# Optimization experiments

Hardware: AMD Instinct MI355X
Metric: run time of the kernel (lower is better)

## Reference

```python
import jax, jax.numpy as jnp
import numpy as np
from jax import lax

B, V_ECC, V_ERR, T, C = 8192, 16, 12, 25, 32
F_IN = C * T           # 800 = temporal_out * tf_num
G = 64                 # gcn_out
H2 = 256               # hidden_size * 2
EHR_DIM, EHR_OUT = 64, 64

def _lhat(V):
    # bidirectional ring graph; PyG ChebConv sym-norm with lambda_max=2.0:
    # L_hat = (2/lmax) * (I - D^-1/2 A D^-1/2) - I = -D^-1/2 A D^-1/2
    i = np.arange(V)
    src = np.concatenate([i, (i + 1) % V])
    dst = np.concatenate([(i + 1) % V, i])
    A = np.zeros((V, V), np.float32)
    A[src, dst] = 1.0
    deg = A.sum(1)
    dinv = np.where(deg > 0, deg ** -0.5, 0.0).astype(np.float32)
    return jnp.asarray(-(dinv[:, None] * A * dinv[None, :]))

LHAT_ECC = _lhat(V_ECC)
LHAT_ERR = _lhat(V_ERR)

def setup_inputs():
    key = jax.random.key(0)
    ks = jax.random.split(key, 23)
    n = lambda k, s: jax.random.normal(k, s, jnp.float32) * 0.02
    return {
        "ecc": jax.random.normal(ks[0], (B, V_ECC, T), jnp.float32),
        "err": jax.random.normal(ks[1], (B, V_ERR, T), jnp.float32),
        "ehr": jax.random.normal(ks[2], (B, EHR_DIM), jnp.float32),
        "wt_ecc": n(ks[3], (C, 1, 3)), "bt_ecc": n(ks[4], (C,)),
        "wt_err": n(ks[5], (C, 1, 3)), "bt_err": n(ks[6], (C,)),
        "W0_ecc": n(ks[7], (F_IN, G)), "W1_ecc": n(ks[8], (F_IN, G)), "b_ecc": n(ks[9], (G,)),
        "W0_err": n(ks[10], (F_IN, G)), "W1_err": n(ks[11], (F_IN, G)), "b_err": n(ks[12], (G,)),
        "Wp_ecc": n(ks[13], (V_ECC * G, H2)), "bp_ecc": n(ks[14], (H2,)),
        "Wp_err": n(ks[15], (V_ERR * G, H2)), "bp_err": n(ks[16], (H2,)),
        "Wa": n(ks[17], (H2, 1)), "ba": n(ks[18], (1,)),
        "We": n(ks[19], (EHR_DIM, EHR_OUT)), "be": n(ks[20], (EHR_OUT,)),
        "Wf2": n(ks[21], (H2 + EHR_OUT, 1)), "bf2": n(ks[22], (1,)),
    }

def _temporal(x, w, b):
    # x: [B, V, T]; Conv1d(1 -> C, k=3, padding=1) per node, then flatten (C, T)
    bb, v, t = x.shape
    y = lax.conv_general_dilated(x.reshape(bb * v, 1, t), w, (1,), "SAME",
                                 dimension_numbers=("NCH", "OIH", "NCH"))
    y = y + b[None, :, None]
    return y.reshape(bb, v, -1)        # [B, V, C*T]

def _cheb(x, lhat, w0, w1, b):
    # K=2 ChebConv: out = T0(x)@W0 + T1(x)@W1 + b, T1 = L_hat x (batched over B)
    tx1 = jnp.einsum("uv,bvd->bud", lhat, x)
    return x @ w0 + tx1 @ w1 + b

def reference(ecc, err, ehr, wt_ecc, bt_ecc, wt_err, bt_err,
              W0_ecc, W1_ecc, b_ecc, W0_err, W1_err, b_err,
              Wp_ecc, bp_ecc, Wp_err, bp_err, Wa, ba, We, be, Wf2, bf2):
    bsz = ecc.shape[0]
    ecc_f = _temporal(ecc, wt_ecc, bt_ecc)                    # [B,16,800]
    err_f = _temporal(err, wt_err, bt_err)                    # [B,12,800]
    ecc_out = _cheb(ecc_f, LHAT_ECC, W0_ecc, W1_ecc, b_ecc)   # [B,16,64]
    err_out = _cheb(err_f, LHAT_ERR, W0_err, W1_err, b_err)   # [B,12,64]
    ecc_g = ecc_out.reshape(bsz, -1) @ Wp_ecc + bp_ecc        # [B,256]
    err_g = err_out.reshape(bsz, -1) @ Wp_err + bp_err        # [B,256]
    attn = jax.nn.sigmoid(jnp.tanh(ecc_g + err_g) @ Wa + ba)  # [B,1]
    fused = attn * ecc_g + (1.0 - attn) * err_g
    ehr_p = jax.nn.relu(ehr @ We + be)                        # dropout = identity (eval)
    combined = jnp.concatenate([fused, ehr_p], axis=1)        # [B,320]
    x = jax.nn.relu(combined)
    return jax.nn.sigmoid(x @ Wf2 + bf2)                      # [B,1]
```

## Files before the change

kernel.cpp:

```cpp
#include <hip/hip_runtime.h>
#include <math.h>

#define B_TOT 8192
#define KE 400
#define KR 300
#define MEP 416
#define MRP 320

#define ROWS 16

#define SXE_LD 424
#define SXR_LD 328
#define SEH_LD 72
#define A_BYTES (ROWS * (SXE_LD + SXR_LD + SEH_LD) * 2)

#define OFF_BE 0
#define OFF_BR 4096
#define U_AET 14336
#define U_ART (U_AET + 256 * MEP)
#define U_WET (U_ART + 256 * MRP)

typedef __attribute__((ext_vector_type(8))) short short8;
typedef __attribute__((ext_vector_type(4))) float floatx4;

__device__ __forceinline__ float sigmoidf_(float x) { return 1.f / (1.f + __expf(-x)); }
__device__ __forceinline__ float tanhf_(float x) { float e = __expf(2.f * x); return (e - 1.f) / (e + 1.f); }
__device__ __forceinline__ unsigned short f2bf(float x) {
    unsigned u = __float_as_uint(x);
    u += 0x7fffu + ((u >> 16) & 1u);
    return (unsigned short)(u >> 16);
}
__device__ __forceinline__ void gload_lds16(const unsigned short* g, unsigned short* l) {
    __builtin_amdgcn_global_load_lds(
        (const __attribute__((address_space(1))) void*)g,
        (__attribute__((address_space(3))) void*)l, 16, 0, 0);
}

__global__ __launch_bounds__(256) void fold_all2(
    const float* __restrict__ wt_ecc, const float* __restrict__ bt_ecc,
    const float* __restrict__ wt_err, const float* __restrict__ bt_err,
    const float* __restrict__ W0_ecc, const float* __restrict__ W1_ecc, const float* __restrict__ b_ecc,
    const float* __restrict__ W0_err, const float* __restrict__ W1_err, const float* __restrict__ b_err,
    const float* __restrict__ Wp_ecc, const float* __restrict__ bp_ecc,
    const float* __restrict__ Wp_err, const float* __restrict__ bp_err,
    const float* __restrict__ We,
    float* __restrict__ wsf, unsigned short* __restrict__ wsu)
{
    const int blk = blockIdx.x;
    const int tid = threadIdx.x;
    const int cq = tid >> 6;
    const int g  = tid & 63;

    __shared__ float red0[4][64];
    __shared__ float red1[4][64];
    __shared__ float sw0[64];
    __shared__ float sw1[64];

    if (blk < MEP + MRP) {
        const int kb = (blk & 7) * 92 + (blk >> 3);
        const bool is_err = (kb >= MEP);
        const int k  = is_err ? kb - MEP : kb;
        const int KK = is_err ? KR : KE;
        const int MP = is_err ? MRP : MEP;
        const int nv = is_err ? 12 : 16;
        const float* wt = is_err ? wt_err : wt_ecc;
        const float* W0 = is_err ? W0_err : W0_ecc;
        const float* W1 = is_err ? W1_err : W1_ecc;
        const float* Wp = is_err ? Wp_err : Wp_ecc;
        const int ubase = is_err ? U_ART : U_AET;

        float s = 0.f;
        if (k < KK) {
            const int v = k / 25, tin = k % 25;
            const int t0 = tin > 0 ? tin - 1 : 0;
            const int t1 = tin < 24 ? tin + 1 : 24;
            float s0 = 0.f, s1 = 0.f;
            #pragma unroll
            for (int c8 = 0; c8 < 8; ++c8) {
                const int c = cq * 8 + c8;
                for (int t = t0; t <= t1; ++t) {
                    const int kk = tin - t + 1;
                    const float w = wt[c * 3 + kk];
                    const int ct = (c * 25 + t) * 64 + g;
                    s0 = fmaf(w, W0[ct], s0);
                    s1 = fmaf(w, W1[ct], s1);
                }
            }
            red0[cq][g] = s0;
            red1[cq][g] = s1;
            __syncthreads();
            if (tid < 64)
                sw0[g] = red0[0][g] + red0[1][g] + red0[2][g] + red0[3][g];
            else if (tid < 128)
                sw1[tid - 64] = red1[0][tid - 64] + red1[1][tid - 64] + red1[2][tid - 64] + red1[3][tid - 64];
            __syncthreads();

            const int vp = (v + 1) % nv;
            const int vm = (v + nv - 1) % nv;
            const int h = tid;
            #pragma unroll 4
            for (int gg = 0; gg < 64; ++gg) {
                s = fmaf(sw0[gg], Wp[(v * 64 + gg) * 256 + h], s);
                s = fmaf(-0.5f * sw1[gg], Wp[(vp * 64 + gg) * 256 + h] + Wp[(vm * 64 + gg) * 256 + h], s);
            }
        }
        wsu[ubase + (size_t)tid * MP + k] = f2bf(s);
    } else if (blk < MEP + MRP + 28) {
        const int cb = blk - (MEP + MRP);
        const bool is_err = (cb >= 16);
        const int i = is_err ? cb - 16 : cb;
        const float* bt = is_err ? bt_err : bt_ecc;
        const float* W0 = is_err ? W0_err : W0_ecc;
        const float* W1 = is_err ? W1_err : W1_ecc;
        const float* bb = is_err ? b_err : b_ecc;
        const float* Wp = is_err ? Wp_err : Wp_ecc;
        const float* bp = is_err ? bp_err : bp_ecc;

        float s = 0.f;
        #pragma unroll
        for (int c8 = 0; c8 < 8; ++c8) {
            const int c = cq * 8 + c8;
            const float btc = bt[c];
            #pragma unroll
            for (int t = 0; t < 25; ++t) {
                const int ct = (c * 25 + t) * 64 + g;
                s = fmaf(btc, W0[ct] - W1[ct], s);
            }
        }
        red0[cq][g] = s;
        __syncthreads();
        if (tid < 64)
            sw0[g] = bb[g] + red0[0][g] + red0[1][g] + red0[2][g] + red0[3][g];
        __syncthreads();

        const int h = tid;
        float p = (i == 0) ? bp[h] : 0.f;
        #pragma unroll 4
        for (int jj = 0; jj < 64; ++jj) {
            const int j = i * 64 + jj;
            p = fmaf(sw0[j & 63], Wp[(size_t)j * 256 + h], p);
        }
        wsf[(is_err ? OFF_BR : OFF_BE) + i * 256 + h] = p;
    } else {
        for (int it = 0; it < 16; ++it) {
            const int idx = it * 256 + tid;
            const int e = idx >> 6, d = idx & 63;
            wsu[U_WET + e * 64 + d] = f2bf(We[d * 64 + e]);
        }
    }
}

__global__ __launch_bounds__(256, 2) void fused_main(
    const float* __restrict__ ecc, const float* __restrict__ err, const float* __restrict__ ehr,
    const float* __restrict__ wsf, const unsigned short* __restrict__ wsu,
    const float* __restrict__ Wa, const float* __restrict__ ba,
    const float* __restrict__ be_, const float* __restrict__ Wf2, const float* __restrict__ bf2,
    float* __restrict__ out)
{
    const unsigned short* awt_e = wsu + U_AET;
    const unsigned short* awt_r = wsu + U_ART;
    const unsigned short* wet   = wsu + U_WET;
    const float* biasE = wsf + OFF_BE;
    const float* biasR = wsf + OFF_BR;

    __shared__ __align__(16) char smem[A_BYTES + 3 * 16384];
    unsigned short* sxe = (unsigned short*)smem;
    unsigned short* sxr = sxe + ROWS * SXE_LD;
    unsigned short* seh = sxr + ROWS * SXR_LD;
    unsigned short* bbuf = (unsigned short*)(smem + A_BYTES);
    float* pa_part = (float*)smem;
    float* at_arr  = pa_part + 64;
    float* po_part = at_arr + 16;

    const int tid = threadIdx.x;
    const int row0 = blockIdx.x * ROWS;
    const int wv = tid >> 6, lane = tid & 63;
    const int lm = lane & 15, lq = lane >> 4;
    const int n0 = wv * 64;

    const int srow = lane >> 2;
    const int scol = ((lane & 3) ^ ((lane >> 3) & 3)) * 8;
    const unsigned short* geb = awt_e + (size_t)(n0 + srow) * MEP + scol;
    const unsigned short* grb = awt_r + (size_t)(n0 + srow) * MRP + scol;

    {
        unsigned short* ld0 = bbuf + 0 * 8192 + wv * 2048;
        unsigned short* ld1 = bbuf + 1 * 8192 + wv * 2048;
        #pragma unroll
        for (int j = 0; j < 4; ++j) {
            gload_lds16(geb + (size_t)j * 16 * MEP + 0 * 32, ld0 + j * 512);
            gload_lds16(geb + (size_t)j * 16 * MEP + 1 * 32, ld1 + j * 512);
        }
    }

    for (int it = 0; it < 7; ++it) {
        const int f = it * 256 + tid;
        if (f < ROWS * 106) {
            const int r = f / 106, q = f - r * 106;
            float4 v = make_float4(0.f, 0.f, 0.f, 0.f);
            if (q < 100) v = *(const float4*)(ecc + (size_t)(row0 + r) * KE + q * 4);
            const unsigned p0 = (unsigned)f2bf(v.x) | ((unsigned)f2bf(v.y) << 16);
            const unsigned p1 = (unsigned)f2bf(v.z) | ((unsigned)f2bf(v.w) << 16);
            *(uint2*)&sxe[r * SXE_LD + q * 4] = make_uint2(p0, p1);
        }
    }
    for (int it = 0; it < 6; ++it) {
        const int f = it * 256 + tid;
        if (f < ROWS * 82) {
            const int r = f / 82, q = f - r * 82;
            float4 v = make_float4(0.f, 0.f, 0.f, 0.f);
            if (q < 75) v = *(const float4*)(err + (size_t)(row0 + r) * KR + q * 4);
            const unsigned p0 = (unsigned)f2bf(v.x) | ((unsigned)f2bf(v.y) << 16);
            const unsigned p1 = (unsigned)f2bf(v.z) | ((unsigned)f2bf(v.w) << 16);
            *(uint2*)&sxr[r * SXR_LD + q * 4] = make_uint2(p0, p1);
        }
    }
    {
        const int r = tid >> 4, q = tid & 15;
        const float4 v = *(const float4*)(ehr + (size_t)(row0 + r) * 64 + q * 4);
        const unsigned p0 = (unsigned)f2bf(v.x) | ((unsigned)f2bf(v.y) << 16);
        const unsigned p1 = (unsigned)f2bf(v.z) | ((unsigned)f2bf(v.w) << 16);
        *(uint2*)&seh[r * SEH_LD + q * 4] = make_uint2(p0, p1);
    }
    __syncthreads();

    floatx4 accE[4], accR[4], accH;
    accH = (floatx4){0.f, 0.f, 0.f, 0.f};
    #pragma unroll
    for (int nt = 0; nt < 4; ++nt) {
        accE[nt] = (floatx4){0.f, 0.f, 0.f, 0.f};
        accR[nt] = (floatx4){0.f, 0.f, 0.f, 0.f};
    }

    #pragma unroll
    for (int kc = 0; kc < 2; ++kc) {
        const short8 b = *(const short8*)(wet + (wv * 16 + lm) * 64 + kc * 32 + lq * 8);
        const short8 a = *(const short8*)&seh[lm * SEH_LD + kc * 32 + lq * 8];
        accH = __builtin_amdgcn_mfma_f32_16x16x32_bf16(a, b, accH, 0, 0, 0);
    }

    const int rswz = (lq ^ ((lm >> 1) & 3)) * 8;
    #pragma unroll
    for (int kc = 0; kc < 23; ++kc) {
        if (kc <= 20) {
            const int c = kc + 2;
            unsigned short* ld = bbuf + (size_t)(c % 3) * 8192 + wv * 2048;
            if (c < 13) {
                #pragma unroll
                for (int j = 0; j < 4; ++j)
                    gload_lds16(geb + (size_t)j * 16 * MEP + c * 32, ld + j * 512);
            } else {
                #pragma unroll
                for (int j = 0; j < 4; ++j)
                    gload_lds16(grb + (size_t)j * 16 * MRP + (c - 13) * 32, ld + j * 512);
            }
            asm volatile("s_waitcnt vmcnt(8)" ::: "memory");
        } else if (kc == 21) {
            asm volatile("s_waitcnt vmcnt(4)" ::: "memory");
        } else {
            asm volatile("s_waitcnt vmcnt(0)" ::: "memory");
        }
        __builtin_amdgcn_sched_barrier(0);

        const unsigned short* slab = bbuf + (size_t)(kc % 3) * 8192 + wv * 2048;
        if (kc < 13) {
            const short8 a0 = *(const short8*)&sxe[lm * SXE_LD + kc * 32 + lq * 8];
            #pragma unroll
            for (int nt = 0; nt < 4; ++nt) {
                const short8 b = *(const short8*)(slab + (nt * 16 + lm) * 32 + rswz);
                accE[nt] = __builtin_amdgcn_mfma_f32_16x16x32_bf16(a0, b, accE[nt], 0, 0, 0);
            }
        } else {
            const short8 a0 = *(const short8*)&sxr[lm * SXR_LD + (kc - 13) * 32 + lq * 8];
            #pragma unroll
            for (int nt = 0; nt < 4; ++nt) {
                const short8 b = *(const short8*)(slab + (nt * 16 + lm) * 32 + rswz);
                accR[nt] = __builtin_amdgcn_mfma_f32_16x16x32_bf16(a0, b, accR[nt], 0, 0, 0);
            }
        }
    }

    float bE[4] = {0.f, 0.f, 0.f, 0.f}, bR[4] = {0.f, 0.f, 0.f, 0.f};
    float wa[4], wf[4];
    #pragma unroll
    for (int i = 0; i < 16; ++i)
        #pragma unroll
        for (int nt = 0; nt < 4; ++nt)
            bE[nt] += biasE[i * 256 + n0 + nt * 16 + lm];
    #pragma unroll
    for (int i = 0; i < 12; ++i)
        #pragma unroll
        for (int nt = 0; nt < 4; ++nt)
            bR[nt] += biasR[i * 256 + n0 + nt * 16 + lm];
    #pragma unroll
    for (int nt = 0; nt < 4; ++nt) {
        const int h = n0 + nt * 16 + lm;
        wa[nt] = Wa[h]; wf[nt] = Wf2[h];
    }
    const int e_lane = wv * 16 + lm;
    const float eh_be = be_[e_lane];
    const float eh_wf = Wf2[256 + e_lane];

    float pa_lane[4];
    #pragma unroll
    for (int rg = 0; rg < 4; ++rg) {
        float s = 0.f;
        #pragma unroll
        for (int nt = 0; nt < 4; ++nt) {
            const float ev = accE[nt][rg] + bE[nt];
            const float rv = accR[nt][rg] + bR[nt];
            s = fmaf(tanhf_(ev + rv), wa[nt], s);
        }
        s += __shfl_xor(s, 1, 64); s += __shfl_xor(s, 2, 64);
        s += __shfl_xor(s, 4, 64); s += __shfl_xor(s, 8, 64);
        pa_lane[rg] = s;
    }

    __syncthreads();
    if (lm == 0) {
        #pragma unroll
        for (int rg = 0; rg < 4; ++rg)
            pa_part[wv * 16 + lq * 4 + rg] = pa_lane[rg];
    }
    __syncthreads();
    if (tid < 16)
        at_arr[tid] = sigmoidf_(pa_part[tid] + pa_part[16 + tid] + pa_part[32 + tid] + pa_part[48 + tid] + ba[0]);
    __syncthreads();

    float po_lane[4];
    #pragma unroll
    for (int rg = 0; rg < 4; ++rg) {
        const int r = lq * 4 + rg;
        const float at = at_arr[r];
        const float om = 1.f - at;
        float s = 0.f;
        #pragma unroll
        for (int nt = 0; nt < 4; ++nt) {
            const float ev = accE[nt][rg] + bE[nt];
            const float rv = accR[nt][rg] + bR[nt];
            s = fmaf(fmaxf(at * ev + om * rv, 0.f), wf[nt], s);
        }
        s = fmaf(fmaxf(accH[rg] + eh_be, 0.f), eh_wf, s);
        s += __shfl_xor(s, 1, 64); s += __shfl_xor(s, 2, 64);
        s += __shfl_xor(s, 4, 64); s += __shfl_xor(s, 8, 64);
        po_lane[rg] = s;
    }
    if (lm == 0) {
        #pragma unroll
        for (int rg = 0; rg < 4; ++rg)
            po_part[wv * 16 + lq * 4 + rg] = po_lane[rg];
    }
    __syncthreads();
    if (tid < 16)
        out[row0 + tid] = sigmoidf_(po_part[tid] + po_part[16 + tid] + po_part[32 + tid] + po_part[48 + tid] + bf2[0]);
}

extern "C" void kernel_launch(void* const* d_in, const int* in_sizes, int n_in,
                              void* d_out, int out_size, void* d_ws, size_t ws_size,
                              hipStream_t stream)
{
    (void)in_sizes; (void)n_in; (void)out_size; (void)ws_size;
    const float* ecc    = (const float*)d_in[0];
    const float* err    = (const float*)d_in[1];
    const float* ehr    = (const float*)d_in[2];
    const float* wt_ecc = (const float*)d_in[3];
    const float* bt_ecc = (const float*)d_in[4];
    const float* wt_err = (const float*)d_in[5];
    const float* bt_err = (const float*)d_in[6];
    const float* W0_ecc = (const float*)d_in[7];
    const float* W1_ecc = (const float*)d_in[8];
    const float* b_ecc  = (const float*)d_in[9];
    const float* W0_err = (const float*)d_in[10];
    const float* W1_err = (const float*)d_in[11];
    const float* b_err  = (const float*)d_in[12];
    const float* Wp_ecc = (const float*)d_in[13];
    const float* bp_ecc = (const float*)d_in[14];
    const float* Wp_err = (const float*)d_in[15];
    const float* bp_err = (const float*)d_in[16];
    const float* Wa     = (const float*)d_in[17];
    const float* ba     = (const float*)d_in[18];
    const float* We     = (const float*)d_in[19];
    const float* be     = (const float*)d_in[20];
    const float* Wf2    = (const float*)d_in[21];
    const float* bf2    = (const float*)d_in[22];
    float* wsf = (float*)d_ws;
    unsigned short* wsu = (unsigned short*)d_ws;
    float* out = (float*)d_out;

    fold_all2<<<dim3(MEP + MRP + 28 + 1), dim3(256), 0, stream>>>(
        wt_ecc, bt_ecc, wt_err, bt_err,
        W0_ecc, W1_ecc, b_ecc, W0_err, W1_err, b_err,
        Wp_ecc, bp_ecc, Wp_err, bp_err, We, wsf, wsu);
    fused_main<<<dim3(B_TOT / ROWS), dim3(256), 0, stream>>>(
        ecc, err, ehr, wsf, wsu, Wa, ba, be, Wf2, bf2, out);
}
```

Baseline: 140.6 us.

## Double rows per block to 32 with 8 waves splitting N

Each block now handles 32 batch rows with 512 threads. Each of the 8 waves computes a 32x32 output tile (two M tiles by two N tiles) instead of a 16x64 tile. Every folded-weight B fragment staged into LDS is reused across two row tiles, which halves the total weight traffic from L2 across the grid. The cost is that each block now runs as a single larger workgroup with more LDS for activations. The EHR branch runs only on the first four waves, and the cross-wave reductions now sum eight partials.

```diff
diff --git a/kernel.cpp b/kernel.cpp
--- a/kernel.cpp
+++ b/kernel.cpp
@@ -7,7 +7,7 @@
 #define MEP 416
 #define MRP 320
 
-#define ROWS 16
+#define ROWS 32
 
 #define SXE_LD 424
 #define SXR_LD 328
@@ -150,7 +150,7 @@
     }
 }
 
-__global__ __launch_bounds__(256, 2) void fused_main(
+__global__ __launch_bounds__(512, 1) void fused_main(
     const float* __restrict__ ecc, const float* __restrict__ err, const float* __restrict__ ehr,
     const float* __restrict__ wsf, const unsigned short* __restrict__ wsu,
     const float* __restrict__ Wa, const float* __restrict__ ba,
@@ -169,32 +169,30 @@
     unsigned short* seh = sxr + ROWS * SXR_LD;
     unsigned short* bbuf = (unsigned short*)(smem + A_BYTES);
     float* pa_part = (float*)smem;
-    float* at_arr  = pa_part + 64;
-    float* po_part = at_arr + 16;
+    float* at_arr  = pa_part + 256;
+    float* po_part = at_arr + 32;
 
     const int tid = threadIdx.x;
     const int row0 = blockIdx.x * ROWS;
     const int wv = tid >> 6, lane = tid & 63;
     const int lm = lane & 15, lq = lane >> 4;
-    const int n0 = wv * 64;
+    const int n0 = wv * 32;
 
     const int srow = lane >> 2;
     const int scol = ((lane & 3) ^ ((lane >> 3) & 3)) * 8;
     const unsigned short* geb = awt_e + (size_t)(n0 + srow) * MEP + scol;
     const unsigned short* grb = awt_r + (size_t)(n0 + srow) * MRP + scol;
 
-    {
-        unsigned short* ld0 = bbuf + 0 * 8192 + wv * 2048;
-        unsigned short* ld1 = bbuf + 1 * 8192 + wv * 2048;
-        #pragma unroll
-        for (int j = 0; j < 4; ++j) {
-            gload_lds16(geb + (size_t)j * 16 * MEP + 0 * 32, ld0 + j * 512);
-            gload_lds16(geb + (size_t)j * 16 * MEP + 1 * 32, ld1 + j * 512);
-        }
+    #pragma unroll
+    for (int c = 0; c < 2; ++c) {
+        unsigned short* ld = bbuf + c * 8192 + wv * 1024;
+        #pragma unroll
+        for (int j = 0; j < 2; ++j)
+            gload_lds16(geb + (size_t)j * 16 * MEP + c * 32, ld + j * 512);
     }
 
     for (int it = 0; it < 7; ++it) {
-        const int f = it * 256 + tid;
+        const int f = it * 512 + tid;
         if (f < ROWS * 106) {
             const int r = f / 106, q = f - r * 106;
             float4 v = make_float4(0.f, 0.f, 0.f, 0.f);
@@ -205,7 +203,7 @@
         }
     }
     for (int it = 0; it < 6; ++it) {
-        const int f = it * 256 + tid;
+        const int f = it * 512 + tid;
         if (f < ROWS * 82) {
             const int r = f / 82, q = f - r * 82;
             float4 v = make_float4(0.f, 0.f, 0.f, 0.f);
@@ -224,19 +222,27 @@
     }
     __syncthreads();
 
-    floatx4 accE[4], accR[4], accH;
-    accH = (floatx4){0.f, 0.f, 0.f, 0.f};
-    #pragma unroll
-    for (int nt = 0; nt < 4; ++nt) {
-        accE[nt] = (floatx4){0.f, 0.f, 0.f, 0.f};
-        accR[nt] = (floatx4){0.f, 0.f, 0.f, 0.f};
-    }
-
-    #pragma unroll
-    for (int kc = 0; kc < 2; ++kc) {
-        const short8 b = *(const short8*)(wet + (wv * 16 + lm) * 64 + kc * 32 + lq * 8);
-        const short8 a = *(const short8*)&seh[lm * SEH_LD + kc * 32 + lq * 8];
-        accH = __builtin_amdgcn_mfma_f32_16x16x32_bf16(a, b, accH, 0, 0, 0);
+    floatx4 accE[2][2], accR[2][2], accH[2];
+    #pragma unroll
+    for (int mt = 0; mt < 2; ++mt) {
+        accH[mt] = (floatx4){0.f, 0.f, 0.f, 0.f};
+        #pragma unroll
+        for (int nt = 0; nt < 2; ++nt) {
+            accE[mt][nt] = (floatx4){0.f, 0.f, 0.f, 0.f};
+            accR[mt][nt] = (floatx4){0.f, 0.f, 0.f, 0.f};
+        }
+    }
+
+    if (wv < 4) {
+        #pragma unroll
+        for (int kc = 0; kc < 2; ++kc) {
+            const short8 b = *(const short8*)(wet + (wv * 16 + lm) * 64 + kc * 32 + lq * 8);
+            #pragma unroll
+            for (int mt = 0; mt < 2; ++mt) {
+                const short8 a = *(const short8*)&seh[(mt * 16 + lm) * SEH_LD + kc * 32 + lq * 8];
+                accH[mt] = __builtin_amdgcn_mfma_f32_16x16x32_bf16(a, b, accH[mt], 0, 0, 0);
+            }
+        }
     }
 
     const int rswz = (lq ^ ((lm >> 1) & 3)) * 8;
@@ -244,115 +250,136 @@
     for (int kc = 0; kc < 23; ++kc) {
         if (kc <= 20) {
             const int c = kc + 2;
-            unsigned short* ld = bbuf + (size_t)(c % 3) * 8192 + wv * 2048;
+            unsigned short* ld = bbuf + (size_t)(c % 3) * 8192 + wv * 1024;
             if (c < 13) {
                 #pragma unroll
-                for (int j = 0; j < 4; ++j)
+                for (int j = 0; j < 2; ++j)
                     gload_lds16(geb + (size_t)j * 16 * MEP + c * 32, ld + j * 512);
             } else {
                 #pragma unroll
-                for (int j = 0; j < 4; ++j)
+                for (int j = 0; j < 2; ++j)
                     gload_lds16(grb + (size_t)j * 16 * MRP + (c - 13) * 32, ld + j * 512);
             }
-            asm volatile("s_waitcnt vmcnt(8)" ::: "memory");
+            asm volatile("s_waitcnt vmcnt(4)" ::: "memory");
         } else if (kc == 21) {
-            asm volatile("s_waitcnt vmcnt(4)" ::: "memory");
+            asm volatile("s_waitcnt vmcnt(2)" ::: "memory");
         } else {
             asm volatile("s_waitcnt vmcnt(0)" ::: "memory");
         }
         __builtin_amdgcn_sched_barrier(0);
 
-        const unsigned short* slab = bbuf + (size_t)(kc % 3) * 8192 + wv * 2048;
+        const unsigned short* slab = bbuf + (size_t)(kc % 3) * 8192 + wv * 1024;
         if (kc < 13) {
             const short8 a0 = *(const short8*)&sxe[lm * SXE_LD + kc * 32 + lq * 8];
-            #pragma unroll
-            for (int nt = 0; nt < 4; ++nt) {
+            const short8 a1 = *(const short8*)&sxe[(16 + lm) * SXE_LD + kc * 32 + lq * 8];
+            #pragma unroll
+            for (int nt = 0; nt < 2; ++nt) {
                 const short8 b = *(const short8*)(slab + (nt * 16 + lm) * 32 + rswz);
-                accE[nt] = __builtin_amdgcn_mfma_f32_16x16x32_bf16(a0, b, accE[nt], 0, 0, 0);
+                accE[0][nt] = __builtin_amdgcn_mfma_f32_16x16x32_bf16(a0, b, accE[0][nt], 0, 0, 0);
+                accE[1][nt] = __builtin_amdgcn_mfma_f32_16x16x32_bf16(a1, b, accE[1][nt], 0, 0, 0);
             }
         } else {
             const short8 a0 = *(const short8*)&sxr[lm * SXR_LD + (kc - 13) * 32 + lq * 8];
-            #pragma unroll
-            for (int nt = 0; nt < 4; ++nt) {
+            const short8 a1 = *(const short8*)&sxr[(16 + lm) * SXR_LD + (kc - 13) * 32 + lq * 8];
+            #pragma unroll
+            for (int nt = 0; nt < 2; ++nt) {
                 const short8 b = *(const short8*)(slab + (nt * 16 + lm) * 32 + rswz);
-                accR[nt] = __builtin_amdgcn_mfma_f32_16x16x32_bf16(a0, b, accR[nt], 0, 0, 0);
-            }
-        }
-    }
-
-    float bE[4] = {0.f, 0.f, 0.f, 0.f}, bR[4] = {0.f, 0.f, 0.f, 0.f};
-    float wa[4], wf[4];
+                accR[0][nt] = __builtin_amdgcn_mfma_f32_16x16x32_bf16(a0, b, accR[0][nt], 0, 0, 0);
+                accR[1][nt] = __builtin_amdgcn_mfma_f32_16x16x32_bf16(a1, b, accR[1][nt], 0, 0, 0);
+            }
+        }
+    }
+
+    float bE[2] = {0.f, 0.f}, bR[2] = {0.f, 0.f};
+    float wa[2], wf[2];
     #pragma unroll
     for (int i = 0; i < 16; ++i)
         #pragma unroll
-        for (int nt = 0; nt < 4; ++nt)
+        for (int nt = 0; nt < 2; ++nt)
             bE[nt] += biasE[i * 256 + n0 + nt * 16 + lm];
     #pragma unroll
     for (int i = 0; i < 12; ++i)
         #pragma unroll
-        for (int nt = 0; nt < 4; ++nt)
+        for (int nt = 0; nt < 2; ++nt)
             bR[nt] += biasR[i * 256 + n0 + nt * 16 + lm];
     #pragma unroll
-    for (int nt = 0; nt < 4; ++nt) {
+    for (int nt = 0; nt < 2; ++nt) {
         const int h = n0 + nt * 16 + lm;
         wa[nt] = Wa[h]; wf[nt] = Wf2[h];
     }
-    const int e_lane = wv * 16 + lm;
+    const int e_lane = (wv & 3) * 16 + lm;
     const float eh_be = be_[e_lane];
     const float eh_wf = Wf2[256 + e_lane];
 
-    float pa_lane[4];
-    #pragma unroll
-    for (int rg = 0; rg < 4; ++rg) {
-        float s = 0.f;
-        #pragma unroll
-        for (int nt = 0; nt < 4; ++nt) {
-            const float ev = accE[nt][rg] + bE[nt];
-            const float rv = accR[nt][rg] + bR[nt];
-            s = fmaf(tanhf_(ev + rv), wa[nt], s);
-        }
-        s += __shfl_xor(s, 1, 64); s += __shfl_xor(s, 2, 64);
-        s += __shfl_xor(s, 4, 64); s += __shfl_xor(s, 8, 64);
-        pa_lane[rg] = s;
-    }
+    float pa_lane[2][4];
+    #pragma unroll
+    for (int mt = 0; mt < 2; ++mt)
+        #pragma unroll
+        for (int rg = 0; rg < 4; ++rg) {
+            float s = 0.f;
+            #pragma unroll
+            for (int nt = 0; nt < 2; ++nt) {
+                const float ev = accE[mt][nt][rg] + bE[nt];
+                const float rv = accR[mt][nt][rg] + bR[nt];
+                s = fmaf(tanhf_(ev + rv), wa[nt], s);
+            }
+            s += __shfl_xor(s, 1, 64); s += __shfl_xor(s, 2, 64);
+            s += __shfl_xor(s, 4, 64); s += __shfl_xor(s, 8, 64);
+            pa_lane[mt][rg] = s;
+        }
 
     __syncthreads();
     if (lm == 0) {
         #pragma unroll
-        for (int rg = 0; rg < 4; ++rg)
-            pa_part[wv * 16 + lq * 4 + rg] = pa_lane[rg];
+        for (int mt = 0; mt < 2; ++mt)
+            #pragma unroll
+            for (int rg = 0; rg < 4; ++rg)
+                pa_part[wv * 32 + mt * 16 + lq * 4 + rg] = pa_lane[mt][rg];
     }
     __syncthreads();
-    if (tid < 16)
-        at_arr[tid] = sigmoidf_(pa_part[tid] + pa_part[16 + tid] + pa_part[32 + tid] + pa_part[48 + tid] + ba[0]);
+    if (tid < 32) {
+        float t = ba[0];
+        #pragma unroll
+        for (int w = 0; w < 8; ++w) t += pa_part[w * 32 + tid];
+        at_arr[tid] = sigmoidf_(t);
+    }
     __syncthreads();
 
-    float po_lane[4];
-    #pragma unroll
-    for (int rg = 0; rg < 4; ++rg) {
-        const int r = lq * 4 + rg;
-        const float at = at_arr[r];
-        const float om = 1.f - at;
-        float s = 0.f;
-        #pragma unroll
-        for (int nt = 0; nt < 4; ++nt) {
-            const float ev = accE[nt][rg] + bE[nt];
-            const float rv = accR[nt][rg] + bR[nt];
-            s = fmaf(fmaxf(at * ev + om * rv, 0.f), wf[nt], s);
-        }
-        s = fmaf(fmaxf(accH[rg] + eh_be, 0.f), eh_wf, s);
-        s += __shfl_xor(s, 1, 64); s += __shfl_xor(s, 2, 64);
-        s += __shfl_xor(s, 4, 64); s += __shfl_xor(s, 8, 64);
-        po_lane[rg] = s;
-    }
+    float po_lane[2][4];
+    #pragma unroll
+    for (int mt = 0; mt < 2; ++mt)
+        #pragma unroll
+        for (int rg = 0; rg < 4; ++rg) {
+            const int r = mt * 16 + lq * 4 + rg;
+            const float at = at_arr[r];
+            const float om = 1.f - at;
+            float s = 0.f;
+            #pragma unroll
+            for (int nt = 0; nt < 2; ++nt) {
+                const float ev = accE[mt][nt][rg] + bE[nt];
+                const float rv = accR[mt][nt][rg] + bR[nt];
+                s = fmaf(fmaxf(at * ev + om * rv, 0.f), wf[nt], s);
+            }
+            if (wv < 4)
+                s = fmaf(fmaxf(accH[mt][rg] + eh_be, 0.f), eh_wf, s);
+            s += __shfl_xor(s, 1, 64); s += __shfl_xor(s, 2, 64);
+            s += __shfl_xor(s, 4, 64); s += __shfl_xor(s, 8, 64);
+            po_lane[mt][rg] = s;
+        }
     if (lm == 0) {
         #pragma unroll
-        for (int rg = 0; rg < 4; ++rg)
-            po_part[wv * 16 + lq * 4 + rg] = po_lane[rg];
+        for (int mt = 0; mt < 2; ++mt)
+            #pragma unroll
+            for (int rg = 0; rg < 4; ++rg)
+                po_part[wv * 32 + mt * 16 + lq * 4 + rg] = po_lane[mt][rg];
     }
     __syncthreads();
-    if (tid < 16)
-        out[row0 + tid] = sigmoidf_(po_part[tid] + po_part[16 + tid] + po_part[32 + tid] + po_part[48 + tid] + bf2[0]);
+    if (tid < 32) {
+        float t = bf2[0];
+        #pragma unroll
+        for (int w = 0; w < 8; ++w) t += po_part[w * 32 + tid];
+        out[row0 + tid] = sigmoidf_(t);
+    }
 }
 
 extern "C" void kernel_launch(void* const* d_in, const int* in_sizes, int n_in,
@@ -391,6 +418,6 @@
         wt_ecc, bt_ecc, wt_err, bt_err,
         W0_ecc, W1_ecc, b_ecc, W0_err, W1_err, b_err,
         Wp_ecc, bp_ecc, Wp_err, bp_err, We, wsf, wsu);
-    fused_main<<<dim3(B_TOT / ROWS), dim3(256), 0, stream>>>(
+    fused_main<<<dim3(B_TOT / ROWS), dim3(512), 0, stream>>>(
         ecc, err, ehr, wsf, wsu, Wa, ba, be, Wf2, bf2, out);
 }
```

Result: faster. 137.8 us, median of 2 (-2.0%).
